# Kernel optimization log

Hardware: AMD Instinct MI355X
Metric: run time of the kernel (lower is better)

The kernel has to match this reference:

```python
import jax, jax.numpy as jnp
import numpy as np

N, E, H, C = 50000, 800000, 4, 32   # nodes, edges, heads, per-head channels
HID, LAT, G = H * C, 32, 128        # hidden, latent, num graphs
IN_DIM = 64
NEG_SLOPE = 0.2
BN_EPS = 1e-5


def setup_inputs() -> dict:
    key = jax.random.key(0)
    ks = jax.random.split(key, 20)
    inp = {
        "x": jax.random.normal(ks[0], (N, IN_DIM), jnp.float32),
        "edge_index": jax.random.randint(ks[1], (2, E), 0, N, jnp.int32),
        "batch": jnp.sort(jax.random.randint(ks[2], (N,), 0, G, jnp.int32)),
        # layer 0
        "W0": jax.random.normal(ks[3], (IN_DIM, HID), jnp.float32) * (1.0 / np.sqrt(IN_DIM)),
        "a_src0": jax.random.normal(ks[4], (H, C), jnp.float32) * 0.1,
        "a_dst0": jax.random.normal(ks[5], (H, C), jnp.float32) * 0.1,
        "b0": jnp.zeros((HID,), jnp.float32),
        # layer 1
        "W1": jax.random.normal(ks[6], (HID, HID), jnp.float32) * (1.0 / np.sqrt(HID)),
        "a_src1": jax.random.normal(ks[7], (H, C), jnp.float32) * 0.1,
        "a_dst1": jax.random.normal(ks[8], (H, C), jnp.float32) * 0.1,
        "b1": jnp.zeros((HID,), jnp.float32),
        # layer 2
        "W2": jax.random.normal(ks[9], (HID, HID), jnp.float32) * (1.0 / np.sqrt(HID)),
        "a_src2": jax.random.normal(ks[10], (H, C), jnp.float32) * 0.1,
        "a_dst2": jax.random.normal(ks[11], (H, C), jnp.float32) * 0.1,
        "b2": jnp.zeros((HID,), jnp.float32),
        # head
        "fc_w": jax.random.normal(ks[12], (HID, LAT), jnp.float32) * (1.0 / np.sqrt(HID)),
        "fc_b": jnp.zeros((LAT,), jnp.float32),
        "bn_g": jnp.ones((LAT,), jnp.float32),
        "bn_b": jnp.zeros((LAT,), jnp.float32),
    }
    return inp


def _gat_conv(x, src, dst, W, a_src, a_dst, b):
    n = x.shape[0]
    h = (x @ W).reshape(n, H, C)                      # [N,H,C]
    alpha_s = jnp.einsum("nhc,hc->nh", h, a_src)       # [N,H]
    alpha_d = jnp.einsum("nhc,hc->nh", h, a_dst)
    e = jax.nn.leaky_relu(alpha_s[src] + alpha_d[dst], NEG_SLOPE)  # [E',H]
    # scatter-softmax over incoming edges of each dst node
    m = jax.ops.segment_max(e, dst, num_segments=n)
    m = jnp.where(jnp.isfinite(m), m, 0.0)
    ex = jnp.exp(e - m[dst])
    denom = jax.ops.segment_sum(ex, dst, num_segments=n)
    alpha = ex / (denom[dst] + 1e-16)                  # [E',H]
    out = jax.ops.segment_sum(alpha[:, :, None] * h[src], dst, num_segments=n)
    return out.reshape(n, H * C) + b


def reference(x, edge_index, batch, W0, a_src0, a_dst0, b0, W1, a_src1, a_dst1, b1,
              W2, a_src2, a_dst2, b2, fc_w, fc_b, bn_g, bn_b):
    # PyG GATConv default add_self_loops=True
    loop = jnp.arange(N, dtype=edge_index.dtype)
    src = jnp.concatenate([edge_index[0], loop])
    dst = jnp.concatenate([edge_index[1], loop])

    h = x
    for (W, a_s, a_d, b) in ((W0, a_src0, a_dst0, b0),
                             (W1, a_src1, a_dst1, b1),
                             (W2, a_src2, a_dst2, b2)):
        h = _gat_conv(h, src, dst, W, a_s, a_d, b)
        h = jax.nn.leaky_relu(h, NEG_SLOPE)  # dropout is identity in eval

    pooled = jax.ops.segment_sum(h, batch, num_segments=G)  # global_add_pool -> [G,HID]
    out = pooled @ fc_w + fc_b
    # BatchNorm1d in eval mode with running_mean=0, running_var=1
    out = bn_g * out * (1.0 / np.sqrt(1.0 + BN_EPS)) + bn_b
    return out
```

## Files before the change

kernel.cpp:

```cpp
#include <hip/hip_runtime.h>
#include <hip/hip_bf16.h>
#include <float.h>

#define NEG 0.2f

__device__ __forceinline__ float leaky(float x) { return x > 0.0f ? x : NEG * x; }

__device__ __forceinline__ unsigned short f2bf(float f) {
  unsigned x = __float_as_uint(f);
  unsigned r = (x + 0x7fffu + ((x >> 16) & 1u)) >> 16;
  return (unsigned short)r;
}

__device__ __forceinline__ float2 bf2f2(unsigned u) {
  float2 r;
  r.x = __uint_as_float(u << 16);
  r.y = __uint_as_float(u & 0xffff0000u);
  return r;
}

__global__ void zero_kernel(int* __restrict__ p, int n) {
  int i = blockIdx.x * blockDim.x + threadIdx.x;
  int stride = gridDim.x * blockDim.x;
  for (; i < n; i += stride) p[i] = 0;
}

__global__ void count_kernel(const int* __restrict__ ei, int* __restrict__ deg, int E, int N) {
  int i = blockIdx.x * blockDim.x + threadIdx.x;
  if (i >= E + N) return;
  int dst = (i < E) ? ei[E + i] : (i - E);
  atomicAdd(&deg[dst], 1);
}

__global__ __launch_bounds__(1024) void scan_block_kernel(const int* __restrict__ deg,
                                                          int* __restrict__ row_start,
                                                          int* __restrict__ sums, int n) {
  __shared__ int buf[1024];
  int t = threadIdx.x;
  int idx = blockIdx.x * 1024 + t;
  int x = (idx < n) ? deg[idx] : 0;
  int v = x;
  buf[t] = v;
  __syncthreads();
  for (int off = 1; off < 1024; off <<= 1) {
    int a = (t >= off) ? buf[t - off] : 0;
    __syncthreads();
    v += a;
    buf[t] = v;
    __syncthreads();
  }
  if (idx < n) row_start[idx] = v - x;
  if (t == 1023) sums[blockIdx.x] = v;
}

__global__ __launch_bounds__(1024) void scan_sums_kernel(int* __restrict__ sums,
                                                         int* __restrict__ row_start,
                                                         int nch, int n) {
  __shared__ int buf[1024];
  int t = threadIdx.x;
  int x = (t < nch) ? sums[t] : 0;
  int v = x;
  buf[t] = v;
  __syncthreads();
  for (int off = 1; off < 1024; off <<= 1) {
    int a = (t >= off) ? buf[t - off] : 0;
    __syncthreads();
    v += a;
    buf[t] = v;
    __syncthreads();
  }
  if (t < nch) sums[t] = v - x;
  if (t == 1023) row_start[n] = v;
}

__global__ __launch_bounds__(1024) void scan_add_kernel(int* __restrict__ row_start,
                                                        const int* __restrict__ sums, int n) {
  int idx = blockIdx.x * 1024 + threadIdx.x;
  if (idx < n) row_start[idx] += sums[blockIdx.x];
}

__global__ void fill_kernel(const int* __restrict__ ei, int* __restrict__ cursor,
                            const int* __restrict__ row_start, int* __restrict__ csr_src,
                            int* __restrict__ csr_dst, int E, int N) {
  int i = blockIdx.x * blockDim.x + threadIdx.x;
  if (i >= E + N) return;
  int src, dst;
  if (i < E) { src = ei[i]; dst = ei[E + i]; } else { src = dst = i - E; }
  int pos = atomicAdd(&cursor[dst], 1);
  int slot = row_start[dst] + pos;
  csr_src[slot] = src;
  csr_dst[slot] = dst;
}

__global__ __launch_bounds__(256) void gemm_kernel(const float* __restrict__ X,
                                                   const float* __restrict__ W,
                                                   unsigned short* __restrict__ Hb,
                                                   const float* __restrict__ a_src,
                                                   const float* __restrict__ a_dst,
                                                   float* __restrict__ as_arr,
                                                   float* __restrict__ ad_arr,
                                                   int nrows, int K) {
  __shared__ float Xs[64][36];
  __shared__ float Ws[32][132];
  int t = threadIdx.x;
  int row0 = blockIdx.x * 64;
  int tcol = t & 31;
  int trow = t >> 5;
  float acc[8][4];
#pragma unroll
  for (int i = 0; i < 8; ++i)
#pragma unroll
    for (int j = 0; j < 4; ++j) acc[i][j] = 0.0f;

  for (int kb = 0; kb < K; kb += 32) {
#pragma unroll
    for (int p = 0; p < 2; ++p) {
      int flat = t + p * 256;
      int r = flat >> 3;
      int kq = (flat & 7) * 4;
      float4 v = make_float4(0.f, 0.f, 0.f, 0.f);
      int gr = row0 + r;
      if (gr < nrows) v = *(const float4*)(X + (size_t)gr * K + kb + kq);
      *(float4*)(&Xs[r][kq]) = v;
    }
#pragma unroll
    for (int p = 0; p < 4; ++p) {
      int flat = t + p * 256;
      int r = flat >> 5;
      int cq = (flat & 31) * 4;
      float4 v = *(const float4*)(W + (size_t)(kb + r) * 128 + cq);
      *(float4*)(&Ws[r][cq]) = v;
    }
    __syncthreads();
#pragma unroll
    for (int kk = 0; kk < 32; kk += 4) {
      float4 xv[8];
#pragma unroll
      for (int i = 0; i < 8; ++i) xv[i] = *(const float4*)(&Xs[trow + 8 * i][kk]);
#pragma unroll
      for (int q = 0; q < 4; ++q) {
        float4 wv = *(const float4*)(&Ws[kk + q][tcol * 4]);
#pragma unroll
        for (int i = 0; i < 8; ++i) {
          float xq = (q == 0) ? xv[i].x : (q == 1) ? xv[i].y : (q == 2) ? xv[i].z : xv[i].w;
          acc[i][0] += xq * wv.x;
          acc[i][1] += xq * wv.y;
          acc[i][2] += xq * wv.z;
          acc[i][3] += xq * wv.w;
        }
      }
    }
    __syncthreads();
  }

  float4 as4 = *(const float4*)(a_src + tcol * 4);
  float4 ad4 = *(const float4*)(a_dst + tcol * 4);
  float ps[8], pd[8];
#pragma unroll
  for (int i = 0; i < 8; ++i) {
    int r = row0 + trow + 8 * i;
    if (r < nrows) {
      union { unsigned short u[4]; uint2 v; } pk;
      pk.u[0] = f2bf(acc[i][0]);
      pk.u[1] = f2bf(acc[i][1]);
      pk.u[2] = f2bf(acc[i][2]);
      pk.u[3] = f2bf(acc[i][3]);
      *(uint2*)(Hb + (size_t)r * 128 + tcol * 4) = pk.v;
    }
    ps[i] = acc[i][0] * as4.x + acc[i][1] * as4.y + acc[i][2] * as4.z + acc[i][3] * as4.w;
    pd[i] = acc[i][0] * ad4.x + acc[i][1] * ad4.y + acc[i][2] * ad4.z + acc[i][3] * ad4.w;
  }
#pragma unroll
  for (int off = 1; off < 8; off <<= 1) {
#pragma unroll
    for (int i = 0; i < 8; ++i) {
      ps[i] += __shfl_xor(ps[i], off);
      pd[i] += __shfl_xor(pd[i], off);
    }
  }
  if ((tcol & 7) == 0) {
    int head = tcol >> 3;
#pragma unroll
    for (int i = 0; i < 8; ++i) {
      int r = row0 + trow + 8 * i;
      if (r < nrows) {
        as_arr[(size_t)r * 4 + head] = ps[i];
        ad_arr[(size_t)r * 4 + head] = pd[i];
      }
    }
  }
}

__global__ __launch_bounds__(256) void ecomp_kernel(const int* __restrict__ csr_src,
                                                    const int* __restrict__ csr_dst,
                                                    const float* __restrict__ as_arr,
                                                    const float* __restrict__ ad_arr,
                                                    float* __restrict__ earr, int Etot) {
  int i = blockIdx.x * 256 + threadIdx.x;
  if (i >= Etot) return;
  int s = csr_src[i];
  int d = csr_dst[i];
  float4 a = *(const float4*)(as_arr + (size_t)s * 4);
  float4 b = *(const float4*)(ad_arr + (size_t)d * 4);
  float4 e;
  e.x = __expf(fminf(leaky(a.x + b.x), 80.f));
  e.y = __expf(fminf(leaky(a.y + b.y), 80.f));
  e.z = __expf(fminf(leaky(a.z + b.z), 80.f));
  e.w = __expf(fminf(leaky(a.w + b.w), 80.f));
  *(float4*)(earr + (size_t)i * 4) = e;
}

template <int POOL>
__global__ __launch_bounds__(256) void agg_kernel(const unsigned short* __restrict__ Hb,
                                                  const float* __restrict__ earr,
                                                  const int* __restrict__ csr_src,
                                                  const int* __restrict__ row_start,
                                                  const float* __restrict__ bias,
                                                  float* __restrict__ xnext,
                                                  const int* __restrict__ batch,
                                                  float* __restrict__ pooled, int N) {
  int wid = threadIdx.x >> 6;
  int lane = threadIdx.x & 63;
  int n = blockIdx.x * 4 + wid;
  if (n >= N) return;
  int rs = row_start[n], re = row_start[n + 1];
  int head = lane >> 4;

  const unsigned* hp = (const unsigned*)Hb + lane;
  const float* ep = earr + head;
  float denom = 0.f, acc0 = 0.f, acc1 = 0.f;
  int i = rs;
  for (; i + 4 <= re; i += 4) {
    int s0 = csr_src[i], s1 = csr_src[i + 1], s2 = csr_src[i + 2], s3 = csr_src[i + 3];
    float e0 = ep[(size_t)i * 4];
    float e1 = ep[(size_t)(i + 1) * 4];
    float e2 = ep[(size_t)(i + 2) * 4];
    float e3 = ep[(size_t)(i + 3) * 4];
    unsigned u0 = hp[(size_t)s0 * 64];
    unsigned u1 = hp[(size_t)s1 * 64];
    unsigned u2 = hp[(size_t)s2 * 64];
    unsigned u3 = hp[(size_t)s3 * 64];
    denom += (e0 + e1) + (e2 + e3);
    float2 f;
    f = bf2f2(u0); acc0 += e0 * f.x; acc1 += e0 * f.y;
    f = bf2f2(u1); acc0 += e1 * f.x; acc1 += e1 * f.y;
    f = bf2f2(u2); acc0 += e2 * f.x; acc1 += e2 * f.y;
    f = bf2f2(u3); acc0 += e3 * f.x; acc1 += e3 * f.y;
  }
  for (; i < re; ++i) {
    int s0 = csr_src[i];
    float e0 = ep[(size_t)i * 4];
    unsigned u0 = hp[(size_t)s0 * 64];
    float2 f = bf2f2(u0);
    denom += e0;
    acc0 += e0 * f.x;
    acc1 += e0 * f.y;
  }
  float inv = 1.0f / (denom + 1e-16f);
  float2 bv = *(const float2*)(bias + 2 * lane);
  float v0 = leaky(acc0 * inv + bv.x);
  float v1 = leaky(acc1 * inv + bv.y);
  if (POOL) {
    int g = batch[n];
    atomicAdd(&pooled[(size_t)g * 128 + 2 * lane], v0);
    atomicAdd(&pooled[(size_t)g * 128 + 2 * lane + 1], v1);
  } else {
    *(float2*)(xnext + (size_t)n * 128 + 2 * lane) = make_float2(v0, v1);
  }
}

__global__ void head_kernel(const float* __restrict__ pooled, const float* __restrict__ fc_w,
                            const float* __restrict__ fc_b, const float* __restrict__ bn_g,
                            const float* __restrict__ bn_b, float* __restrict__ out, int G) {
  int t = threadIdx.x;
  int g = blockIdx.x * 8 + (t >> 5);
  int j = t & 31;
  if (g >= G) return;
  const float* pr = pooled + (size_t)g * 128;
  float acc = 0.f;
#pragma unroll 8
  for (int k = 0; k < 128; ++k) acc += pr[k] * fc_w[k * 32 + j];
  const float inv = 0.9999950000374997f;
  out[g * 32 + j] = bn_g[j] * (acc + fc_b[j]) * inv + bn_b[j];
}

extern "C" void kernel_launch(void* const* d_in, const int* in_sizes, int n_in,
                              void* d_out, int out_size, void* d_ws, size_t ws_size,
                              hipStream_t stream) {
  const float* x = (const float*)d_in[0];
  const int* ei = (const int*)d_in[1];
  const int* batch = (const int*)d_in[2];
  const float* Wm[3] = {(const float*)d_in[3], (const float*)d_in[7], (const float*)d_in[11]};
  const float* a_s[3] = {(const float*)d_in[4], (const float*)d_in[8], (const float*)d_in[12]};
  const float* a_d[3] = {(const float*)d_in[5], (const float*)d_in[9], (const float*)d_in[13]};
  const float* bb[3] = {(const float*)d_in[6], (const float*)d_in[10], (const float*)d_in[14]};
  const float* fc_w = (const float*)d_in[15];
  const float* fc_b = (const float*)d_in[16];
  const float* bn_g = (const float*)d_in[17];
  const float* bn_b = (const float*)d_in[18];
  float* out = (float*)d_out;

  int N = in_sizes[0] / 64;
  int E = in_sizes[1] / 2;
  int G = out_size / 32;
  int Etot = E + N;

  char* p = (char*)d_ws;
  auto carve = [&](size_t bytes) {
    char* r = p;
    p += (bytes + 255) & ~size_t(255);
    return r;
  };
  int* deg       = (int*)carve((size_t)N * 4);
  int* cursor    = (int*)carve((size_t)N * 4);
  float* pooled  = (float*)carve((size_t)G * 128 * 4);
  int* row_start = (int*)carve((size_t)(N + 1) * 4);
  int* sums      = (int*)carve(4096);
  int* csr_src   = (int*)carve((size_t)Etot * 4);
  int* csr_dst   = (int*)carve((size_t)Etot * 4);
  float* earr    = (float*)carve((size_t)Etot * 4 * 4);
  unsigned short* Hb = (unsigned short*)carve((size_t)N * 128 * 2);
  float* bufX    = (float*)carve((size_t)N * 128 * 4);
  float* as_arr  = (float*)carve((size_t)N * 4 * 4);
  float* ad_arr  = (float*)carve((size_t)N * 4 * 4);

  int nz = (int)(((char*)(pooled + (size_t)G * 128) - (char*)deg) / 4);
  zero_kernel<<<512, 256, 0, stream>>>(deg, nz);

  int egrid = (Etot + 255) / 256;
  count_kernel<<<egrid, 256, 0, stream>>>(ei, deg, E, N);
  int nch = (N + 1023) / 1024;
  scan_block_kernel<<<nch, 1024, 0, stream>>>(deg, row_start, sums, N);
  scan_sums_kernel<<<1, 1024, 0, stream>>>(sums, row_start, nch, N);
  scan_add_kernel<<<nch, 1024, 0, stream>>>(row_start, sums, N);
  fill_kernel<<<egrid, 256, 0, stream>>>(ei, cursor, row_start, csr_src, csr_dst, E, N);

  int ggrid = (N + 63) / 64;
  int ngrid = (N + 3) / 4;

  gemm_kernel<<<ggrid, 256, 0, stream>>>(x, Wm[0], Hb, a_s[0], a_d[0], as_arr, ad_arr, N, 64);
  ecomp_kernel<<<egrid, 256, 0, stream>>>(csr_src, csr_dst, as_arr, ad_arr, earr, Etot);
  agg_kernel<0><<<ngrid, 256, 0, stream>>>(Hb, earr, csr_src, row_start, bb[0],
                                           bufX, nullptr, nullptr, N);
  gemm_kernel<<<ggrid, 256, 0, stream>>>(bufX, Wm[1], Hb, a_s[1], a_d[1], as_arr, ad_arr, N, 128);
  ecomp_kernel<<<egrid, 256, 0, stream>>>(csr_src, csr_dst, as_arr, ad_arr, earr, Etot);
  agg_kernel<0><<<ngrid, 256, 0, stream>>>(Hb, earr, csr_src, row_start, bb[1],
                                           bufX, nullptr, nullptr, N);
  gemm_kernel<<<ggrid, 256, 0, stream>>>(bufX, Wm[2], Hb, a_s[2], a_d[2], as_arr, ad_arr, N, 128);
  ecomp_kernel<<<egrid, 256, 0, stream>>>(csr_src, csr_dst, as_arr, ad_arr, earr, Etot);
  agg_kernel<1><<<ngrid, 256, 0, stream>>>(Hb, earr, csr_src, row_start, bb[2],
                                           nullptr, batch, pooled, N);

  head_kernel<<<(G + 7) / 8, 256, 0, stream>>>(pooled, fc_w, fc_b, bn_g, bn_b, out, G);
}
```

Measured before the change: 483.1 us.

## Use bf16 MFMA GEMM, store bf16 activations, and bucket CSR fill by source range

The FP32 SIMT GEMM becomes a bf16 MFMA 16x16x32 kernel. The whole X tile and transposed W sit in LDS, and the bf16 output is staged through LDS for coalesced stores. Intermediate activations between layers are now stored as bf16, which halves their traffic, and a conversion kernel turns the input x into bf16. The CSR fill runs in several passes, one per 8192-node source range, so each destination row ends up grouped by source for better gather locality. The cost is extra launches that each re-read the full edge list, plus lower precision in the activations.

```diff
diff --git a/kernel.cpp b/kernel.cpp
--- a/kernel.cpp
+++ b/kernel.cpp
@@ -19,10 +19,18 @@
   return r;
 }
 
+using frag8 = __attribute__((ext_vector_type(8))) short;
+using f32x4v = __attribute__((ext_vector_type(4))) float;
+
 __global__ void zero_kernel(int* __restrict__ p, int n) {
   int i = blockIdx.x * blockDim.x + threadIdx.x;
   int stride = gridDim.x * blockDim.x;
   for (; i < n; i += stride) p[i] = 0;
+}
+
+__global__ void xcvt_kernel(const float* __restrict__ x, unsigned short* __restrict__ xb, int n) {
+  int i = blockIdx.x * blockDim.x + threadIdx.x;
+  if (i < n) xb[i] = f2bf(x[i]);
 }
 
 __global__ void count_kernel(const int* __restrict__ ei, int* __restrict__ deg, int E, int N) {
@@ -81,18 +89,19 @@
 
 __global__ void fill_kernel(const int* __restrict__ ei, int* __restrict__ cursor,
                             const int* __restrict__ row_start, int* __restrict__ csr_src,
-                            int* __restrict__ csr_dst, int E, int N) {
+                            int* __restrict__ csr_dst, int E, int N, int rpass) {
   int i = blockIdx.x * blockDim.x + threadIdx.x;
   if (i >= E + N) return;
   int src, dst;
   if (i < E) { src = ei[i]; dst = ei[E + i]; } else { src = dst = i - E; }
+  if ((src >> 13) != rpass) return;
   int pos = atomicAdd(&cursor[dst], 1);
   int slot = row_start[dst] + pos;
   csr_src[slot] = src;
   csr_dst[slot] = dst;
 }
 
-__global__ __launch_bounds__(256) void gemm_kernel(const float* __restrict__ X,
+__global__ __launch_bounds__(256) void gemm_kernel(const unsigned short* __restrict__ Xb,
                                                    const float* __restrict__ W,
                                                    unsigned short* __restrict__ Hb,
                                                    const float* __restrict__ a_src,
@@ -100,94 +109,87 @@
                                                    float* __restrict__ as_arr,
                                                    float* __restrict__ ad_arr,
                                                    int nrows, int K) {
-  __shared__ float Xs[64][36];
-  __shared__ float Ws[32][132];
+  __shared__ unsigned short Wt[128][136];
+  __shared__ unsigned short Xs[64][136];
   int t = threadIdx.x;
-  int row0 = blockIdx.x * 64;
-  int tcol = t & 31;
-  int trow = t >> 5;
-  float acc[8][4];
-#pragma unroll
-  for (int i = 0; i < 8; ++i)
-#pragma unroll
-    for (int j = 0; j < 4; ++j) acc[i][j] = 0.0f;
+  int wave = t >> 6, lane = t & 63;
+  int n0 = lane & 15, quad = lane >> 4;
+  int row0 = blockIdx.x * 64, wrow = wave * 16;
+
+  for (int idx = t; idx < K * 128; idx += 256) {
+    int k = idx >> 7, n = idx & 127;
+    Wt[n][k] = f2bf(W[idx]);
+  }
+  int rowElems = K >> 3;
+  for (int idx = t; idx < 64 * rowElems; idx += 256) {
+    int r = idx / rowElems, c8 = idx % rowElems;
+    int gr = row0 + r;
+    uint4 v = make_uint4(0, 0, 0, 0);
+    if (gr < nrows) v = *(const uint4*)(Xb + (size_t)gr * K + c8 * 8);
+    *(uint4*)(&Xs[r][c8 * 8]) = v;
+  }
+  __syncthreads();
+
+  f32x4v acc[8];
+#pragma unroll
+  for (int c = 0; c < 8; ++c) acc[c] = (f32x4v){0.f, 0.f, 0.f, 0.f};
 
   for (int kb = 0; kb < K; kb += 32) {
-#pragma unroll
-    for (int p = 0; p < 2; ++p) {
-      int flat = t + p * 256;
-      int r = flat >> 3;
-      int kq = (flat & 7) * 4;
-      float4 v = make_float4(0.f, 0.f, 0.f, 0.f);
-      int gr = row0 + r;
-      if (gr < nrows) v = *(const float4*)(X + (size_t)gr * K + kb + kq);
-      *(float4*)(&Xs[r][kq]) = v;
+    frag8 a = *(const frag8*)(&Xs[wrow + n0][kb + quad * 8]);
+#pragma unroll
+    for (int c = 0; c < 8; ++c) {
+      frag8 b = *(const frag8*)(&Wt[c * 16 + n0][kb + quad * 8]);
+      acc[c] = __builtin_amdgcn_mfma_f32_16x16x32_bf16(a, b, acc[c], 0, 0, 0);
     }
-#pragma unroll
-    for (int p = 0; p < 4; ++p) {
-      int flat = t + p * 256;
-      int r = flat >> 5;
-      int cq = (flat & 31) * 4;
-      float4 v = *(const float4*)(W + (size_t)(kb + r) * 128 + cq);
-      *(float4*)(&Ws[r][cq]) = v;
+  }
+
+  float asv[8], adv[8];
+#pragma unroll
+  for (int c = 0; c < 8; ++c) {
+    asv[c] = a_src[c * 16 + n0];
+    adv[c] = a_dst[c * 16 + n0];
+  }
+#pragma unroll
+  for (int r = 0; r < 4; ++r) {
+    float ps[4] = {0.f, 0.f, 0.f, 0.f}, pd[4] = {0.f, 0.f, 0.f, 0.f};
+#pragma unroll
+    for (int c = 0; c < 8; ++c) {
+      int h = c >> 1;
+      ps[h] += acc[c][r] * asv[c];
+      pd[h] += acc[c][r] * adv[c];
     }
-    __syncthreads();
-#pragma unroll
-    for (int kk = 0; kk < 32; kk += 4) {
-      float4 xv[8];
-#pragma unroll
-      for (int i = 0; i < 8; ++i) xv[i] = *(const float4*)(&Xs[trow + 8 * i][kk]);
-#pragma unroll
-      for (int q = 0; q < 4; ++q) {
-        float4 wv = *(const float4*)(&Ws[kk + q][tcol * 4]);
-#pragma unroll
-        for (int i = 0; i < 8; ++i) {
-          float xq = (q == 0) ? xv[i].x : (q == 1) ? xv[i].y : (q == 2) ? xv[i].z : xv[i].w;
-          acc[i][0] += xq * wv.x;
-          acc[i][1] += xq * wv.y;
-          acc[i][2] += xq * wv.z;
-          acc[i][3] += xq * wv.w;
+#pragma unroll
+    for (int off = 1; off < 16; off <<= 1) {
+#pragma unroll
+      for (int h = 0; h < 4; ++h) {
+        ps[h] += __shfl_xor(ps[h], off);
+        pd[h] += __shfl_xor(pd[h], off);
+      }
+    }
+    if (n0 == 0) {
+      int m = row0 + wrow + quad * 4 + r;
+      if (m < nrows) {
+#pragma unroll
+        for (int h = 0; h < 4; ++h) {
+          as_arr[(size_t)m * 4 + h] = ps[h];
+          ad_arr[(size_t)m * 4 + h] = pd[h];
         }
       }
     }
-    __syncthreads();
-  }
-
-  float4 as4 = *(const float4*)(a_src + tcol * 4);
-  float4 ad4 = *(const float4*)(a_dst + tcol * 4);
-  float ps[8], pd[8];
-#pragma unroll
-  for (int i = 0; i < 8; ++i) {
-    int r = row0 + trow + 8 * i;
-    if (r < nrows) {
-      union { unsigned short u[4]; uint2 v; } pk;
-      pk.u[0] = f2bf(acc[i][0]);
-      pk.u[1] = f2bf(acc[i][1]);
-      pk.u[2] = f2bf(acc[i][2]);
-      pk.u[3] = f2bf(acc[i][3]);
-      *(uint2*)(Hb + (size_t)r * 128 + tcol * 4) = pk.v;
-    }
-    ps[i] = acc[i][0] * as4.x + acc[i][1] * as4.y + acc[i][2] * as4.z + acc[i][3] * as4.w;
-    pd[i] = acc[i][0] * ad4.x + acc[i][1] * ad4.y + acc[i][2] * ad4.z + acc[i][3] * ad4.w;
-  }
-#pragma unroll
-  for (int off = 1; off < 8; off <<= 1) {
-#pragma unroll
-    for (int i = 0; i < 8; ++i) {
-      ps[i] += __shfl_xor(ps[i], off);
-      pd[i] += __shfl_xor(pd[i], off);
-    }
-  }
-  if ((tcol & 7) == 0) {
-    int head = tcol >> 3;
-#pragma unroll
-    for (int i = 0; i < 8; ++i) {
-      int r = row0 + trow + 8 * i;
-      if (r < nrows) {
-        as_arr[(size_t)r * 4 + head] = ps[i];
-        ad_arr[(size_t)r * 4 + head] = pd[i];
-      }
-    }
+  }
+
+  __syncthreads();
+#pragma unroll
+  for (int c = 0; c < 8; ++c)
+#pragma unroll
+    for (int r = 0; r < 4; ++r)
+      Xs[wrow + quad * 4 + r][c * 16 + n0] = f2bf(acc[c][r]);
+  __syncthreads();
+  for (int idx = t; idx < 64 * 16; idx += 256) {
+    int r = idx >> 4, c8 = idx & 15;
+    int gr = row0 + r;
+    if (gr < nrows)
+      *(uint4*)(Hb + (size_t)gr * 128 + c8 * 8) = *(const uint4*)(&Xs[r][c8 * 8]);
   }
 }
 
@@ -216,7 +218,7 @@
                                                   const int* __restrict__ csr_src,
                                                   const int* __restrict__ row_start,
                                                   const float* __restrict__ bias,
-                                                  float* __restrict__ xnext,
+                                                  unsigned short* __restrict__ xnext,
                                                   const int* __restrict__ batch,
                                                   float* __restrict__ pooled, int N) {
   int wid = threadIdx.x >> 6;
@@ -265,7 +267,8 @@
     atomicAdd(&pooled[(size_t)g * 128 + 2 * lane], v0);
     atomicAdd(&pooled[(size_t)g * 128 + 2 * lane + 1], v1);
   } else {
-    *(float2*)(xnext + (size_t)n * 128 + 2 * lane) = make_float2(v0, v1);
+    unsigned pk = ((unsigned)f2bf(v1) << 16) | (unsigned)f2bf(v0);
+    ((unsigned*)xnext)[(size_t)n * 64 + lane] = pk;
   }
 }
 
@@ -320,12 +323,14 @@
   int* csr_dst   = (int*)carve((size_t)Etot * 4);
   float* earr    = (float*)carve((size_t)Etot * 4 * 4);
   unsigned short* Hb = (unsigned short*)carve((size_t)N * 128 * 2);
-  float* bufX    = (float*)carve((size_t)N * 128 * 4);
+  unsigned short* Xb = (unsigned short*)carve((size_t)N * 128 * 2);
   float* as_arr  = (float*)carve((size_t)N * 4 * 4);
   float* ad_arr  = (float*)carve((size_t)N * 4 * 4);
 
   int nz = (int)(((char*)(pooled + (size_t)G * 128) - (char*)deg) / 4);
   zero_kernel<<<512, 256, 0, stream>>>(deg, nz);
+
+  xcvt_kernel<<<(N * 64 + 255) / 256, 256, 0, stream>>>(x, Xb, N * 64);
 
   int egrid = (Etot + 255) / 256;
   count_kernel<<<egrid, 256, 0, stream>>>(ei, deg, E, N);
@@ -333,20 +338,22 @@
   scan_block_kernel<<<nch, 1024, 0, stream>>>(deg, row_start, sums, N);
   scan_sums_kernel<<<1, 1024, 0, stream>>>(sums, row_start, nch, N);
   scan_add_kernel<<<nch, 1024, 0, stream>>>(row_start, sums, N);
-  fill_kernel<<<egrid, 256, 0, stream>>>(ei, cursor, row_start, csr_src, csr_dst, E, N);
+  int npass = ((N - 1) >> 13) + 1;
+  for (int r = 0; r < npass; ++r)
+    fill_kernel<<<egrid, 256, 0, stream>>>(ei, cursor, row_start, csr_src, csr_dst, E, N, r);
 
   int ggrid = (N + 63) / 64;
   int ngrid = (N + 3) / 4;
 
-  gemm_kernel<<<ggrid, 256, 0, stream>>>(x, Wm[0], Hb, a_s[0], a_d[0], as_arr, ad_arr, N, 64);
+  gemm_kernel<<<ggrid, 256, 0, stream>>>(Xb, Wm[0], Hb, a_s[0], a_d[0], as_arr, ad_arr, N, 64);
   ecomp_kernel<<<egrid, 256, 0, stream>>>(csr_src, csr_dst, as_arr, ad_arr, earr, Etot);
   agg_kernel<0><<<ngrid, 256, 0, stream>>>(Hb, earr, csr_src, row_start, bb[0],
-                                           bufX, nullptr, nullptr, N);
-  gemm_kernel<<<ggrid, 256, 0, stream>>>(bufX, Wm[1], Hb, a_s[1], a_d[1], as_arr, ad_arr, N, 128);
+                                           Xb, nullptr, nullptr, N);
+  gemm_kernel<<<ggrid, 256, 0, stream>>>(Xb, Wm[1], Hb, a_s[1], a_d[1], as_arr, ad_arr, N, 128);
   ecomp_kernel<<<egrid, 256, 0, stream>>>(csr_src, csr_dst, as_arr, ad_arr, earr, Etot);
   agg_kernel<0><<<ngrid, 256, 0, stream>>>(Hb, earr, csr_src, row_start, bb[1],
-                                           bufX, nullptr, nullptr, N);
-  gemm_kernel<<<ggrid, 256, 0, stream>>>(bufX, Wm[2], Hb, a_s[2], a_d[2], as_arr, ad_arr, N, 128);
+                                           Xb, nullptr, nullptr, N);
+  gemm_kernel<<<ggrid, 256, 0, stream>>>(Xb, Wm[2], Hb, a_s[2], a_d[2], as_arr, ad_arr, N, 128);
   ecomp_kernel<<<egrid, 256, 0, stream>>>(csr_src, csr_dst, as_arr, ad_arr, earr, Etot);
   agg_kernel<1><<<ngrid, 256, 0, stream>>>(Hb, earr, csr_src, row_start, bb[2],
                                            nullptr, batch, pooled, N);
```

Result: slower. 495.9 us (+2.6%).
